# Performance work log

Hardware: AMD Instinct MI355X
Metric: run time of the kernel (lower is better)

Reference implementation:

```python
import jax, jax.numpy as jnp
import numpy as np

N_NODES = 50000
DEG = 16
N_EDGES = N_NODES * DEG  # 800000
C_IN = 64
C_OUT = 64


def setup_inputs() -> dict:
    key = jax.random.key(0)
    k_x, k_src, k_ea, k_w, k_b = jax.random.split(key, 5)
    x = jax.random.normal(k_x, (N_NODES, C_IN), dtype=jnp.float32)
    # Every node appears DEG times as a destination -> no empty segments in max-aggregation.
    dst = jnp.repeat(jnp.arange(N_NODES, dtype=jnp.int32), DEG)
    src = jax.random.randint(k_src, (N_EDGES,), 0, N_NODES, dtype=jnp.int32)
    edge_index = jnp.stack([src, dst], axis=0)  # [2, E], row0=source(j), row1=target(i)
    edge_attr = jax.random.normal(k_ea, (N_EDGES, 1), dtype=jnp.float32)  # unused by forward (faithful to source)
    # MLP(2*C_IN -> C_OUT): Linear weight [out, 2*in] + bias, kaiming-ish scale
    W = jax.random.normal(k_w, (C_OUT, 2 * C_IN), dtype=jnp.float32) * (1.0 / np.sqrt(2 * C_IN))
    b = jax.random.normal(k_b, (C_OUT,), dtype=jnp.float32) * 0.01
    return {"x": x, "edge_index": edge_index, "edge_attr": edge_attr, "W": W, "b": b}


def reference(x, edge_index, edge_attr, W, b):
    # PyG EdgeConv: out_i = max_{j in N(i)} MLP(concat(x_i, x_j - x_i)); aggr='max'
    src = edge_index[0]  # j (source)
    dst = edge_index[1]  # i (target)
    x_i = x[dst]                      # [E, C]
    x_j = x[src]                      # [E, C]
    feat = jnp.concatenate([x_i, x_j - x_i], axis=-1)   # [E, 2C]
    msg = jax.nn.relu(feat @ W.T + b)                    # [E, C_out] per-edge MLP
    out = jax.ops.segment_max(msg, dst, num_segments=x.shape[0])  # scatter-max
    # Guard against -inf for isolated nodes (none by construction, but match scatter fill=0)
    return jnp.where(jnp.isneginf(out), 0.0, out)
```

## Files before the change

kernel.cpp:

```cpp
#include <hip/hip_runtime.h>
#include <hip/hip_bf16.h>


#define DEG 16
#define C 64
#define WPB 4

typedef __attribute__((ext_vector_type(8))) short s16x8;
typedef __attribute__((ext_vector_type(4))) float f32x4;

__device__ __forceinline__ unsigned pk2(float lo, float hi) {
    __hip_bfloat162 h = __float22bfloat162_rn(make_float2(lo, hi));
    union { __hip_bfloat162 h; unsigned u; } c; c.h = h;
    return c.u;
}
__device__ __forceinline__ s16x8 cvt_frag(f32x4 a, f32x4 b) {
    union { unsigned u[4]; s16x8 v; } r;
    r.u[0] = pk2(a[0], a[1]); r.u[1] = pk2(a[2], a[3]);
    r.u[2] = pk2(b[0], b[1]); r.u[3] = pk2(b[2], b[3]);
    return r.v;
}
__device__ __forceinline__ float bf2f(unsigned short u) {
    union { unsigned u; float f; } c; c.u = ((unsigned)u) << 16;
    return c.f;
}

__global__ __launch_bounds__(256, 2) void dense_yb(
    const float* __restrict__ x,
    const float* __restrict__ W,
    const float* __restrict__ bias,
    signed char* __restrict__ Y8,
    float* __restrict__ scale,
    unsigned short* __restrict__ Bb,
    int n_groups, int n_nodes)
{
    const int lane = threadIdx.x & 63;
    const int wave = threadIdx.x >> 6;
    const int col  = lane & 15;
    const int quad = lane >> 4;
    int group = blockIdx.x * WPB + wave;
    if (group >= n_groups) group = n_groups - 1;
    const int node0 = group * 16;

    s16x8 bd[4][2], b2[4][2];
    #pragma unroll
    for (int nt = 0; nt < 4; ++nt) {
        const float* wrow = W + (nt * 16 + col) * (2 * C);
        #pragma unroll
        for (int ks = 0; ks < 2; ++ks) {
            const int k0 = ks * 32 + quad * 8;
            f32x4 w1a = *(const f32x4*)(wrow + k0);
            f32x4 w1b = *(const f32x4*)(wrow + k0 + 4);
            f32x4 w2a = *(const f32x4*)(wrow + C + k0);
            f32x4 w2b = *(const f32x4*)(wrow + C + k0 + 4);
            b2[nt][ks] = cvt_frag(w2a, w2b);
            f32x4 da, db;
            #pragma unroll
            for (int j = 0; j < 4; ++j) { da[j] = w1a[j] - w2a[j]; db[j] = w1b[j] - w2b[j]; }
            bd[nt][ks] = cvt_frag(da, db);
        }
    }

    int arow = node0 + col;
    if (arow >= n_nodes) arow = n_nodes - 1;
    const float* xp = x + (size_t)arow * C + quad * 8;
    s16x8 xi0 = cvt_frag(*(const f32x4*)xp, *(const f32x4*)(xp + 4));
    s16x8 xi1 = cvt_frag(*(const f32x4*)(xp + 32), *(const f32x4*)(xp + 36));

    f32x4 yD[4], bD[4];
    #pragma unroll
    for (int nt = 0; nt < 4; ++nt) {
        float bv = bias[nt * 16 + col];
        bD[nt] = (f32x4){bv, bv, bv, bv};
        yD[nt] = (f32x4){0.f, 0.f, 0.f, 0.f};
    }
    #pragma unroll
    for (int nt = 0; nt < 4; ++nt) {
        yD[nt] = __builtin_amdgcn_mfma_f32_16x16x32_bf16(xi0, b2[nt][0], yD[nt], 0, 0, 0);
        yD[nt] = __builtin_amdgcn_mfma_f32_16x16x32_bf16(xi1, b2[nt][1], yD[nt], 0, 0, 0);
        bD[nt] = __builtin_amdgcn_mfma_f32_16x16x32_bf16(xi0, bd[nt][0], bD[nt], 0, 0, 0);
        bD[nt] = __builtin_amdgcn_mfma_f32_16x16x32_bf16(xi1, bd[nt][1], bD[nt], 0, 0, 0);
    }

    #pragma unroll
    for (int r = 0; r < 4; ++r) {
        int row = node0 + quad * 4 + r;
        if (row >= n_nodes) row = n_nodes - 1;
        float am = fmaxf(fmaxf(fabsf(yD[0][r]), fabsf(yD[1][r])),
                         fmaxf(fabsf(yD[2][r]), fabsf(yD[3][r])));
        am = fmaxf(am, __shfl_xor(am, 1));
        am = fmaxf(am, __shfl_xor(am, 2));
        am = fmaxf(am, __shfl_xor(am, 4));
        am = fmaxf(am, __shfl_xor(am, 8));
        const float inv = am > 0.f ? 127.0f / am : 0.f;
        #pragma unroll
        for (int nt = 0; nt < 4; ++nt) {
            int q = __float2int_rn(yD[nt][r] * inv);
            q = q > 127 ? 127 : (q < -127 ? -127 : q);
            Y8[(size_t)row * C + nt * 16 + col] = (signed char)q;
            Bb[(size_t)row * C + nt * 16 + col] =
                (unsigned short)(pk2(bD[nt][r], 0.f) & 0xFFFF);
        }
        if (col == 0) scale[row] = am * (1.0f / 127.0f);
    }
}

__global__ __launch_bounds__(256, 6) void gathermax(
    const signed char* __restrict__ Y8,
    const float* __restrict__ scale,
    const unsigned short* __restrict__ Bb,
    const int* __restrict__ src,
    float* __restrict__ out,
    int n_nodes)
{
    const int lane = threadIdx.x & 63;
    const int wave = threadIdx.x >> 6;
    int i = blockIdx.x * WPB + wave;
    if (i >= n_nodes) i = n_nodes - 1;

    int jreg = 0;
    if (lane < DEG) jreg = src[i * DEG + lane];

    float bs = bf2f(Bb[(size_t)i * C + lane]);

    signed char v[DEG];
    float sc[DEG];
    #pragma unroll
    for (int e = 0; e < DEG; ++e) {
        int j = __shfl(jreg, e);
        v[e]  = Y8[(size_t)j * C + lane];
        sc[e] = scale[j];
    }

    float m = (float)v[0] * sc[0];
    #pragma unroll
    for (int e = 1; e < DEG; ++e) m = fmaxf(m, (float)v[e] * sc[e]);

    out[(size_t)i * C + lane] = fmaxf(bs + m, 0.0f);
}

__global__ __launch_bounds__(256, 2) void edgeconv_fallback(
    const float* __restrict__ x, const int* __restrict__ src,
    const float* __restrict__ W, const float* __restrict__ bias,
    float* __restrict__ out, int n_groups)
{
    const int lane = threadIdx.x & 63, wave = threadIdx.x >> 6;
    const int col = lane & 15, quad = lane >> 4;
    int group = blockIdx.x * WPB + wave;
    if (group >= n_groups) group = n_groups - 1;

    auto frag = [&](int row, int koff) {
        const float* p = x + row * C + koff;
        return cvt_frag(*(const f32x4*)p, *(const f32x4*)(p + 4));
    };

    s16x8 b2[4][2];
    f32x4 baseD[4];
    {
        s16x8 bd[4][2];
        #pragma unroll
        for (int nt = 0; nt < 4; ++nt) {
            const float* wrow = W + (nt * 16 + col) * (2 * C);
            #pragma unroll
            for (int ks = 0; ks < 2; ++ks) {
                const int k0 = ks * 32 + quad * 8;
                f32x4 w1a = *(const f32x4*)(wrow + k0);
                f32x4 w1b = *(const f32x4*)(wrow + k0 + 4);
                f32x4 w2a = *(const f32x4*)(wrow + C + k0);
                f32x4 w2b = *(const f32x4*)(wrow + C + k0 + 4);
                b2[nt][ks] = cvt_frag(w2a, w2b);
                f32x4 da, db;
                #pragma unroll
                for (int j = 0; j < 4; ++j) { da[j] = w1a[j] - w2a[j]; db[j] = w1b[j] - w2b[j]; }
                bd[nt][ks] = cvt_frag(da, db);
            }
        }
        #pragma unroll
        for (int nt = 0; nt < 4; ++nt) {
            float bv = bias[nt * 16 + col];
            baseD[nt] = (f32x4){bv, bv, bv, bv};
        }
        const int nrow = group * 16 + col;
        s16x8 xi0 = frag(nrow, quad * 8), xi1 = frag(nrow, 32 + quad * 8);
        #pragma unroll
        for (int nt = 0; nt < 4; ++nt) {
            baseD[nt] = __builtin_amdgcn_mfma_f32_16x16x32_bf16(xi0, bd[nt][0], baseD[nt], 0, 0, 0);
            baseD[nt] = __builtin_amdgcn_mfma_f32_16x16x32_bf16(xi1, bd[nt][1], baseD[nt], 0, 0, 0);
        }
    }
    int idx[16];
    #pragma unroll
    for (int n = 0; n < 16; ++n) idx[n] = src[group * 256 + n * DEG + col];
    s16x8 xa[3][2];
    #pragma unroll
    for (int p = 0; p < 2; ++p) {
        xa[p][0] = frag(idx[p], quad * 8); xa[p][1] = frag(idx[p], 32 + quad * 8);
    }
    #pragma unroll
    for (int n = 0; n < 16; ++n) {
        if (n + 2 < 16) {
            xa[(n + 2) % 3][0] = frag(idx[n + 2], quad * 8);
            xa[(n + 2) % 3][1] = frag(idx[n + 2], 32 + quad * 8);
        }
        const int slane = ((n >> 2) << 4) | col;
        f32x4 acc[4];
        #pragma unroll
        for (int nt = 0; nt < 4; ++nt) {
            float bb = __shfl(baseD[nt][n & 3], slane);
            acc[nt] = (f32x4){bb, bb, bb, bb};
        }
        #pragma unroll
        for (int nt = 0; nt < 4; ++nt) {
            acc[nt] = __builtin_amdgcn_mfma_f32_16x16x32_bf16(xa[n % 3][0], b2[nt][0], acc[nt], 0, 0, 0);
            acc[nt] = __builtin_amdgcn_mfma_f32_16x16x32_bf16(xa[n % 3][1], b2[nt][1], acc[nt], 0, 0, 0);
        }
        float m[4];
        #pragma unroll
        for (int nt = 0; nt < 4; ++nt) {
            float t = fmaxf(fmaxf(acc[nt][0], acc[nt][1]),
                            fmaxf(acc[nt][2], acc[nt][3]));
            t = fmaxf(t, __shfl_xor(t, 16));
            t = fmaxf(t, __shfl_xor(t, 32));
            m[nt] = t;
        }
        float r = quad == 0 ? m[0] : quad == 1 ? m[1] : quad == 2 ? m[2] : m[3];
        out[(group * 16 + n) * C + lane] = fmaxf(r, 0.0f);
    }
}

extern "C" void kernel_launch(void* const* d_in, const int* in_sizes, int n_in,
                              void* d_out, int out_size, void* d_ws, size_t ws_size,
                              hipStream_t stream) {
    const float* x    = (const float*)d_in[0];
    const int*   src  = (const int*)  d_in[1];
    const float* W    = (const float*)d_in[3];
    const float* b    = (const float*)d_in[4];
    float*       out  = (float*)d_out;

    const int n_nodes = in_sizes[0] / C;

    const size_t y8_bytes = (size_t)n_nodes * C;
    const size_t sc_bytes = (size_t)n_nodes * sizeof(float);
    const size_t bb_bytes = (size_t)n_nodes * C * sizeof(unsigned short);

    if (ws_size >= y8_bytes + sc_bytes + bb_bytes) {
        signed char*    Y8 = (signed char*)d_ws;
        float*          SC = (float*)((char*)d_ws + y8_bytes);
        unsigned short* Bb = (unsigned short*)((char*)d_ws + y8_bytes + sc_bytes);
        const int n_groups = (n_nodes + 15) / 16;
        dense_yb<<<(n_groups + WPB - 1) / WPB, 256, 0, stream>>>(
            x, W, b, Y8, SC, Bb, n_groups, n_nodes);
        gathermax<<<(n_nodes + WPB - 1) / WPB, 256, 0, stream>>>(
            Y8, SC, Bb, src, out, n_nodes);
    } else {
        const int n_groups = (n_nodes + 15) / 16;
        edgeconv_fallback<<<(n_groups + WPB - 1) / WPB, 256, 0, stream>>>(
            x, src, W, b, out, n_groups);
    }
}
```

Measured before the change: 107.5 us.

## Fuse dense and gather-max phases into one cooperative persistent kernel with grid sync

Replaces the two kernel launches with a single cooperative persistent kernel. Each wave grid-strides over node groups for the dense bf16 MFMA phase, performs a grid-wide sync, then grid-strides over nodes for the int8 gather-max phase. The gather phase also prefetches the next node's indices and bias and loads the per-edge scales with one lane-parallel load plus shuffles. The aim is to remove the second launch gap and amortise the weight-fragment setup, at the cost of a grid barrier, an occupancy query on the host, and fewer waves in flight for hiding latency in the gather.

```diff
diff --git a/kernel.cpp b/kernel.cpp
--- a/kernel.cpp
+++ b/kernel.cpp
@@ -1,10 +1,12 @@
 #include <hip/hip_runtime.h>
 #include <hip/hip_bf16.h>
+#include <hip/hip_cooperative_groups.h>
+
+namespace cg = cooperative_groups;
 
 
 #define DEG 16
 #define C 64
-#define WPB 4
 
 typedef __attribute__((ext_vector_type(8))) short s16x8;
 typedef __attribute__((ext_vector_type(4))) float f32x4;
@@ -25,22 +27,16 @@
     return c.f;
 }
 
-__global__ __launch_bounds__(256, 2) void dense_yb(
-    const float* __restrict__ x,
-    const float* __restrict__ W,
+__device__ __forceinline__ void phase1_body(
+    const float* __restrict__ x, const float* __restrict__ W,
     const float* __restrict__ bias,
-    signed char* __restrict__ Y8,
-    float* __restrict__ scale,
+    signed char* __restrict__ Y8, float* __restrict__ SC,
     unsigned short* __restrict__ Bb,
-    int n_groups, int n_nodes)
+    int n_groups, int n_nodes, int gwave, int nwaves)
 {
     const int lane = threadIdx.x & 63;
-    const int wave = threadIdx.x >> 6;
     const int col  = lane & 15;
     const int quad = lane >> 4;
-    int group = blockIdx.x * WPB + wave;
-    if (group >= n_groups) group = n_groups - 1;
-    const int node0 = group * 16;
 
     s16x8 bd[4][2], b2[4][2];
     #pragma unroll
@@ -60,83 +56,130 @@
             bd[nt][ks] = cvt_frag(da, db);
         }
     }
-
-    int arow = node0 + col;
-    if (arow >= n_nodes) arow = n_nodes - 1;
-    const float* xp = x + (size_t)arow * C + quad * 8;
-    s16x8 xi0 = cvt_frag(*(const f32x4*)xp, *(const f32x4*)(xp + 4));
-    s16x8 xi1 = cvt_frag(*(const f32x4*)(xp + 32), *(const f32x4*)(xp + 36));
-
-    f32x4 yD[4], bD[4];
-    #pragma unroll
-    for (int nt = 0; nt < 4; ++nt) {
-        float bv = bias[nt * 16 + col];
-        bD[nt] = (f32x4){bv, bv, bv, bv};
-        yD[nt] = (f32x4){0.f, 0.f, 0.f, 0.f};
-    }
-    #pragma unroll
-    for (int nt = 0; nt < 4; ++nt) {
-        yD[nt] = __builtin_amdgcn_mfma_f32_16x16x32_bf16(xi0, b2[nt][0], yD[nt], 0, 0, 0);
-        yD[nt] = __builtin_amdgcn_mfma_f32_16x16x32_bf16(xi1, b2[nt][1], yD[nt], 0, 0, 0);
-        bD[nt] = __builtin_amdgcn_mfma_f32_16x16x32_bf16(xi0, bd[nt][0], bD[nt], 0, 0, 0);
-        bD[nt] = __builtin_amdgcn_mfma_f32_16x16x32_bf16(xi1, bd[nt][1], bD[nt], 0, 0, 0);
-    }
-
-    #pragma unroll
-    for (int r = 0; r < 4; ++r) {
-        int row = node0 + quad * 4 + r;
-        if (row >= n_nodes) row = n_nodes - 1;
-        float am = fmaxf(fmaxf(fabsf(yD[0][r]), fabsf(yD[1][r])),
-                         fmaxf(fabsf(yD[2][r]), fabsf(yD[3][r])));
-        am = fmaxf(am, __shfl_xor(am, 1));
-        am = fmaxf(am, __shfl_xor(am, 2));
-        am = fmaxf(am, __shfl_xor(am, 4));
-        am = fmaxf(am, __shfl_xor(am, 8));
-        const float inv = am > 0.f ? 127.0f / am : 0.f;
-        #pragma unroll
-        for (int nt = 0; nt < 4; ++nt) {
-            int q = __float2int_rn(yD[nt][r] * inv);
-            q = q > 127 ? 127 : (q < -127 ? -127 : q);
-            Y8[(size_t)row * C + nt * 16 + col] = (signed char)q;
-            Bb[(size_t)row * C + nt * 16 + col] =
-                (unsigned short)(pk2(bD[nt][r], 0.f) & 0xFFFF);
-        }
-        if (col == 0) scale[row] = am * (1.0f / 127.0f);
-    }
-}
-
-__global__ __launch_bounds__(256, 6) void gathermax(
-    const signed char* __restrict__ Y8,
-    const float* __restrict__ scale,
-    const unsigned short* __restrict__ Bb,
-    const int* __restrict__ src,
-    float* __restrict__ out,
-    int n_nodes)
+    float bv[4];
+    #pragma unroll
+    for (int nt = 0; nt < 4; ++nt) bv[nt] = bias[nt * 16 + col];
+
+    for (int group = gwave; group < n_groups; group += nwaves) {
+        const int node0 = group * 16;
+        int arow = node0 + col;
+        if (arow >= n_nodes) arow = n_nodes - 1;
+        const float* xp = x + (size_t)arow * C + quad * 8;
+        s16x8 xi0 = cvt_frag(*(const f32x4*)xp, *(const f32x4*)(xp + 4));
+        s16x8 xi1 = cvt_frag(*(const f32x4*)(xp + 32), *(const f32x4*)(xp + 36));
+
+        f32x4 yD[4], bD[4];
+        #pragma unroll
+        for (int nt = 0; nt < 4; ++nt) {
+            bD[nt] = (f32x4){bv[nt], bv[nt], bv[nt], bv[nt]};
+            yD[nt] = (f32x4){0.f, 0.f, 0.f, 0.f};
+        }
+        #pragma unroll
+        for (int nt = 0; nt < 4; ++nt) {
+            yD[nt] = __builtin_amdgcn_mfma_f32_16x16x32_bf16(xi0, b2[nt][0], yD[nt], 0, 0, 0);
+            yD[nt] = __builtin_amdgcn_mfma_f32_16x16x32_bf16(xi1, b2[nt][1], yD[nt], 0, 0, 0);
+            bD[nt] = __builtin_amdgcn_mfma_f32_16x16x32_bf16(xi0, bd[nt][0], bD[nt], 0, 0, 0);
+            bD[nt] = __builtin_amdgcn_mfma_f32_16x16x32_bf16(xi1, bd[nt][1], bD[nt], 0, 0, 0);
+        }
+
+        #pragma unroll
+        for (int r = 0; r < 4; ++r) {
+            int row = node0 + quad * 4 + r;
+            if (row >= n_nodes) row = n_nodes - 1;
+            float am = fmaxf(fmaxf(fabsf(yD[0][r]), fabsf(yD[1][r])),
+                             fmaxf(fabsf(yD[2][r]), fabsf(yD[3][r])));
+            am = fmaxf(am, __shfl_xor(am, 1));
+            am = fmaxf(am, __shfl_xor(am, 2));
+            am = fmaxf(am, __shfl_xor(am, 4));
+            am = fmaxf(am, __shfl_xor(am, 8));
+            const float inv = am > 0.f ? 127.0f / am : 0.f;
+            #pragma unroll
+            for (int nt = 0; nt < 4; ++nt) {
+                int q = __float2int_rn(yD[nt][r] * inv);
+                q = q > 127 ? 127 : (q < -127 ? -127 : q);
+                Y8[(size_t)row * C + nt * 16 + col] = (signed char)q;
+                Bb[(size_t)row * C + nt * 16 + col] =
+                    (unsigned short)(pk2(bD[nt][r], 0.f) & 0xFFFF);
+            }
+            if (col == 0) SC[row] = am * (1.0f / 127.0f);
+        }
+    }
+}
+
+__device__ __forceinline__ void phase2_body(
+    const signed char* __restrict__ Y8, const float* __restrict__ SC,
+    const unsigned short* __restrict__ Bb, const int* __restrict__ src,
+    float* __restrict__ out, int n_nodes, int gwave, int nwaves)
 {
     const int lane = threadIdx.x & 63;
-    const int wave = threadIdx.x >> 6;
-    int i = blockIdx.x * WPB + wave;
-    if (i >= n_nodes) i = n_nodes - 1;
-
-    int jreg = 0;
-    if (lane < DEG) jreg = src[i * DEG + lane];
-
-    float bs = bf2f(Bb[(size_t)i * C + lane]);
-
-    signed char v[DEG];
-    float sc[DEG];
-    #pragma unroll
-    for (int e = 0; e < DEG; ++e) {
-        int j = __shfl(jreg, e);
-        v[e]  = Y8[(size_t)j * C + lane];
-        sc[e] = scale[j];
-    }
-
-    float m = (float)v[0] * sc[0];
-    #pragma unroll
-    for (int e = 1; e < DEG; ++e) m = fmaxf(m, (float)v[e] * sc[e]);
-
-    out[(size_t)i * C + lane] = fmaxf(bs + m, 0.0f);
+    int i = gwave;
+    if (i >= n_nodes) return;
+
+    int   jreg = (lane < DEG) ? src[i * DEG + lane] : 0;
+    float bs   = bf2f(Bb[(size_t)i * C + lane]);
+    float scl  = (lane < DEG) ? SC[jreg] : 0.f;
+
+    while (true) {
+        const int inext = i + nwaves;
+        int jn = 0; float bn = 0.f;
+        if (inext < n_nodes) {
+            jn = (lane < DEG) ? src[inext * DEG + lane] : 0;
+            bn = bf2f(Bb[(size_t)inext * C + lane]);
+        }
+
+        signed char v[DEG];
+        #pragma unroll
+        for (int e = 0; e < DEG; ++e) {
+            int j = __shfl(jreg, e);
+            v[e] = Y8[(size_t)j * C + lane];
+        }
+        float m = -3.0e38f;
+        #pragma unroll
+        for (int e = 0; e < DEG; ++e) {
+            float s = __shfl(scl, e);
+            m = fmaxf(m, (float)v[e] * s);
+        }
+        out[(size_t)i * C + lane] = fmaxf(bs + m, 0.0f);
+
+        if (inext >= n_nodes) break;
+        i = inext; jreg = jn; bs = bn;
+        scl = (lane < DEG) ? SC[jreg] : 0.f;
+    }
+}
+
+__global__ __launch_bounds__(256, 3) void edgeconv_coop(
+    const float* __restrict__ x, const int* __restrict__ src,
+    const float* __restrict__ W, const float* __restrict__ bias,
+    signed char* __restrict__ Y8, float* __restrict__ SC,
+    unsigned short* __restrict__ Bb, float* __restrict__ out,
+    int n_groups, int n_nodes)
+{
+    const int gwave  = (int)((blockIdx.x * blockDim.x + threadIdx.x) >> 6);
+    const int nwaves = (int)((gridDim.x * blockDim.x) >> 6);
+    phase1_body(x, W, bias, Y8, SC, Bb, n_groups, n_nodes, gwave, nwaves);
+    __threadfence();
+    cg::this_grid().sync();
+    phase2_body(Y8, SC, Bb, src, out, n_nodes, gwave, nwaves);
+}
+
+__global__ __launch_bounds__(256, 3) void k_phase1(
+    const float* __restrict__ x, const float* __restrict__ W,
+    const float* __restrict__ bias, signed char* __restrict__ Y8,
+    float* __restrict__ SC, unsigned short* __restrict__ Bb,
+    int n_groups, int n_nodes)
+{
+    const int gwave  = (int)((blockIdx.x * blockDim.x + threadIdx.x) >> 6);
+    const int nwaves = (int)((gridDim.x * blockDim.x) >> 6);
+    phase1_body(x, W, bias, Y8, SC, Bb, n_groups, n_nodes, gwave, nwaves);
+}
+__global__ __launch_bounds__(256, 6) void k_phase2(
+    const signed char* __restrict__ Y8, const float* __restrict__ SC,
+    const unsigned short* __restrict__ Bb, const int* __restrict__ src,
+    float* __restrict__ out, int n_nodes)
+{
+    const int gwave  = (int)((blockIdx.x * blockDim.x + threadIdx.x) >> 6);
+    const int nwaves = (int)((gridDim.x * blockDim.x) >> 6);
+    phase2_body(Y8, SC, Bb, src, out, n_nodes, gwave, nwaves);
 }
 
 __global__ __launch_bounds__(256, 2) void edgeconv_fallback(
@@ -146,7 +189,7 @@
 {
     const int lane = threadIdx.x & 63, wave = threadIdx.x >> 6;
     const int col = lane & 15, quad = lane >> 4;
-    int group = blockIdx.x * WPB + wave;
+    int group = blockIdx.x * 4 + wave;
     if (group >= n_groups) group = n_groups - 1;
 
     auto frag = [&](int row, int koff) {
@@ -177,8 +220,8 @@
         }
         #pragma unroll
         for (int nt = 0; nt < 4; ++nt) {
-            float bv = bias[nt * 16 + col];
-            baseD[nt] = (f32x4){bv, bv, bv, bv};
+            float bvv = bias[nt * 16 + col];
+            baseD[nt] = (f32x4){bvv, bvv, bvv, bvv};
         }
         const int nrow = group * 16 + col;
         s16x8 xi0 = frag(nrow, quad * 8), xi1 = frag(nrow, 32 + quad * 8);
@@ -238,6 +281,7 @@
     float*       out  = (float*)d_out;
 
     const int n_nodes = in_sizes[0] / C;
+    const int n_groups = (n_nodes + 15) / 16;
 
     const size_t y8_bytes = (size_t)n_nodes * C;
     const size_t sc_bytes = (size_t)n_nodes * sizeof(float);
@@ -247,14 +291,26 @@
         signed char*    Y8 = (signed char*)d_ws;
         float*          SC = (float*)((char*)d_ws + y8_bytes);
         unsigned short* Bb = (unsigned short*)((char*)d_ws + y8_bytes + sc_bytes);
-        const int n_groups = (n_nodes + 15) / 16;
-        dense_yb<<<(n_groups + WPB - 1) / WPB, 256, 0, stream>>>(
-            x, W, b, Y8, SC, Bb, n_groups, n_nodes);
-        gathermax<<<(n_nodes + WPB - 1) / WPB, 256, 0, stream>>>(
-            Y8, SC, Bb, src, out, n_nodes);
+
+        int maxB = 0;
+        hipError_t oe = hipOccupancyMaxActiveBlocksPerMultiprocessor(
+            &maxB, edgeconv_coop, 256, 0);
+        int grid = (oe == hipSuccess && maxB > 0) ? maxB * 256 : 512;
+        if (grid > 1024) grid = 1024;
+
+        void* args[] = {(void*)&x, (void*)&src, (void*)&W, (void*)&b,
+                        (void*)&Y8, (void*)&SC, (void*)&Bb, (void*)&out,
+                        (void*)&n_groups, (void*)&n_nodes};
+        hipError_t e = hipLaunchCooperativeKernel(
+            edgeconv_coop, dim3(grid), dim3(256), args, 0, stream);
+        if (e != hipSuccess) {
+            k_phase1<<<(n_groups + 3) / 4, 256, 0, stream>>>(
+                x, W, b, Y8, SC, Bb, n_groups, n_nodes);
+            k_phase2<<<(n_nodes + 3) / 4, 256, 0, stream>>>(
+                Y8, SC, Bb, src, out, n_nodes);
+        }
     } else {
-        const int n_groups = (n_nodes + 15) / 16;
-        edgeconv_fallback<<<(n_groups + WPB - 1) / WPB, 256, 0, stream>>>(
+        edgeconv_fallback<<<(n_groups + 3) / 4, 256, 0, stream>>>(
             x, src, W, b, out, n_groups);
     }
 }
```

Result: slower. 204.8 us (+90.6%).
